# Optimization experiments

Measured on AMD Instinct MI355X. Metric: run time of the kernel, lower is better.

## Reference

```python
import jax, jax.numpy as jnp
import numpy as np

SEQ, B, IN_DIM, EMB, HID, L = 2048, 32, 512, 256, 256, 16
START, STOP = 0, 1
HH = HID // 2  # per-direction hidden size
NEG = -10000.0


def _lstm_dir(xs, Wih, Whh, b, h0, c0, reverse):
    # xs: (T, B, EMB); Wih: (4*HH, EMB); Whh: (4*HH, HH); b: (4*HH,)
    def step(carry, x):
        h, c = carry
        g = x @ Wih.T + h @ Whh.T + b  # (B, 4*HH)
        i, f, gg, o = jnp.split(g, 4, axis=-1)  # PyTorch gate order i,f,g,o
        c = jax.nn.sigmoid(f) * c + jax.nn.sigmoid(i) * jnp.tanh(gg)
        h = jax.nn.sigmoid(o) * jnp.tanh(c)
        return (h, c), h
    _, hs = jax.lax.scan(step, (h0, c0), xs, reverse=reverse)
    return hs  # (T, B, HH)


def _features(source_seq, in_W, in_b, Wih_f, Whh_f, b_f, Wih_b, Whh_b, b_b,
              out_W, out_b, h0, c0):
    x = source_seq @ in_W.T + in_b  # (T, B, EMB)
    hf = _lstm_dir(x, Wih_f, Whh_f, b_f, h0[0], c0[0], reverse=False)
    hb = _lstm_dir(x, Wih_b, Whh_b, b_b, h0[1], c0[1], reverse=True)
    h = jnp.concatenate([hf, hb], axis=-1)  # (T, B, HID)
    return h @ out_W.T + out_b  # (T, B, L)


def _viterbi(feats, transitions):
    # transitions[i, j]: score of transitioning to label i from label j
    fv = jnp.full((B, L), NEG, feats.dtype).at[:, START].set(0.0)

    def step(fv, feat):
        scores = fv[:, None, :] + transitions[None, :, :]  # (B, next, prev)
        bp = jnp.argmax(scores, axis=2).astype(jnp.int32)   # (B, L)
        fv = jnp.max(scores, axis=2) + feat
        return fv, bp

    fv, bps = jax.lax.scan(step, fv, feats)  # bps: (T, B, L)
    term = fv + transitions[STOP][None, :]   # (B, L)
    score = jnp.max(term, axis=1)            # (B,)
    best_last = jnp.argmax(term, axis=1).astype(jnp.int32)  # (B,)

    def back(lbl, bp):
        prev = jnp.take_along_axis(bp, lbl[:, None], axis=1)[:, 0]
        return prev, lbl

    _, path = jax.lax.scan(back, best_last, bps, reverse=True)  # (T, B)
    return score, path


def setup_inputs() -> dict:
    key = jax.random.key(0)
    ks = jax.random.split(key, 16)
    s = 0.05
    return {
        "source_seq": jax.random.normal(ks[0], (SEQ, B, IN_DIM), jnp.float32),
        "in_W": jax.random.normal(ks[1], (EMB, IN_DIM), jnp.float32) * s,
        "in_b": jnp.zeros((EMB,), jnp.float32),
        "Wih_f": jax.random.normal(ks[2], (4 * HH, EMB), jnp.float32) * s,
        "Whh_f": jax.random.normal(ks[3], (4 * HH, HH), jnp.float32) * s,
        "b_f": jnp.zeros((4 * HH,), jnp.float32),
        "Wih_b": jax.random.normal(ks[4], (4 * HH, EMB), jnp.float32) * s,
        "Whh_b": jax.random.normal(ks[5], (4 * HH, HH), jnp.float32) * s,
        "b_b": jnp.zeros((4 * HH,), jnp.float32),
        "out_W": jax.random.normal(ks[6], (L, HID), jnp.float32) * s,
        "out_b": jnp.zeros((L,), jnp.float32),
        "transitions": jax.random.normal(ks[7], (L, L), jnp.float32),
        "h0": jax.random.normal(ks[8], (2, B, HH), jnp.float32),
        "c0": jax.random.normal(ks[9], (2, B, HH), jnp.float32),
    }


def reference(source_seq, in_W, in_b, Wih_f, Whh_f, b_f, Wih_b, Whh_b, b_b,
              out_W, out_b, transitions, h0, c0):
    feats = _features(source_seq, in_W, in_b, Wih_f, Whh_f, b_f,
                      Wih_b, Whh_b, b_b, out_W, out_b, h0, c0)
    score, labels = _viterbi(feats, transitions)
    return score, labels
```

## Files before the change

### kernel.cpp

```cpp
#include <hip/hip_runtime.h>
#include <hip/hip_bf16.h>

typedef __attribute__((ext_vector_type(8))) short bf16x8;
typedef __attribute__((ext_vector_type(4))) float f32x4;
typedef __attribute__((ext_vector_type(4))) unsigned u32x4;
typedef __attribute__((ext_vector_type(2))) unsigned u32x2;

#define SEQT 2048
#define BATCH 32
#define INDIM 512
#define EMB 256
#define HHX 128
#define LBL 16
#define LOG2E 1.44269504f

__device__ __forceinline__ unsigned short f2bf(float f) {
    unsigned u = __float_as_uint(f);
    u += 0x7FFFu + ((u >> 16) & 1u);
    return (unsigned short)(u >> 16);
}
#define BLO(u) __uint_as_float((u) << 16)
#define BHI(u) __uint_as_float((u) & 0xffff0000u)

__device__ __forceinline__ float cell(float ig, float fg, float gg, float og, float& c) {
    float Ef = __builtin_amdgcn_exp2f(fminf(fg, 30.f));
    float Ei = __builtin_amdgcn_exp2f(fminf(ig, 30.f));
    float Eg = __builtin_amdgcn_exp2f(fminf(gg, 60.f));
    float Eo = __builtin_amdgcn_exp2f(fminf(og, 30.f));
    float pf = 1.f + Ef;
    float t1 = (Eg + 1.f) * (1.f + Ei);
    float num = c * t1 + (Eg - 1.f) * pf;
    float cn = num * __builtin_amdgcn_rcpf(pf * t1);
    c = cn;
    float E2 = __builtin_amdgcn_exp2f(fminf(2.f * LOG2E * cn, 60.f));
    float r3 = __builtin_amdgcn_rcpf((E2 + 1.f) * (1.f + Eo));
    return (E2 - 1.f) * r3;
}

__device__ __forceinline__ int orig_of(int gp) {
    return ((gp >> 4) & 3) * 128 + (gp >> 6) * 16 + (gp & 15);
}
__device__ __forceinline__ float gate_scale(int gp) {
    return (((gp >> 4) & 3) == 2) ? (2.f * LOG2E) : (-LOG2E);
}

__global__ __launch_bounds__(256) void k_prep_wc(
    const float* __restrict__ in_W, const float* __restrict__ in_b,
    const float* __restrict__ Wih_f, const float* __restrict__ b_f,
    const float* __restrict__ Wih_b, const float* __restrict__ b_b,
    unsigned short* __restrict__ Wc, float* __restrict__ bc)
{
    int G0 = blockIdx.x * 8;
    int tid = threadIdx.x;
    __shared__ float wrow[8][EMB];
    for (int e = tid; e < 8 * EMB; e += 256) {
        int r = e >> 8, ee = e & 255;
        int G = G0 + r, dir = G >> 9, gp = G & 511;
        wrow[r][ee] = (dir ? Wih_b : Wih_f)[orig_of(gp) * EMB + ee] * gate_scale(gp);
    }
    __syncthreads();
    for (int k = tid; k < INDIM; k += 256) {
        float acc[8] = {0, 0, 0, 0, 0, 0, 0, 0};
        #pragma unroll 4
        for (int e = 0; e < EMB; ++e) {
            float x = in_W[e * INDIM + k];
            #pragma unroll
            for (int r = 0; r < 8; ++r) acc[r] += wrow[r][e] * x;
        }
        #pragma unroll
        for (int r = 0; r < 8; ++r) Wc[(size_t)(G0 + r) * INDIM + k] = f2bf(acc[r]);
    }
    if (tid < 64) {
        for (int r = 0; r < 8; ++r) {
            float p = 0.f;
            for (int e = tid; e < EMB; e += 64) p += wrow[r][e] * in_b[e];
            for (int off = 32; off; off >>= 1) p += __shfl_xor(p, off);
            if (tid == 0) {
                int G = G0 + r, dir = G >> 9, gp = G & 511;
                bc[G] = (dir ? b_b : b_f)[orig_of(gp)] * gate_scale(gp) + p;
            }
        }
    }
}

__global__ __launch_bounds__(256) void k_prep_misc(
    const float* __restrict__ Whh_f, const float* __restrict__ Whh_b,
    const float* __restrict__ out_W,
    unsigned short* __restrict__ Whh_bf, unsigned short* __restrict__ outW_bf)
{
    int idx = blockIdx.x * 256 + threadIdx.x;
    int stride = gridDim.x * 256;
    for (int i = idx; i < 1024 * HHX; i += stride) {
        int G = i >> 7, k = i & 127;
        int dir = G >> 9, gp = G & 511;
        const float* Whh = dir ? Whh_b : Whh_f;
        Whh_bf[i] = f2bf(Whh[orig_of(gp) * HHX + k] * gate_scale(gp));
    }
    for (int i = idx; i < LBL * 256; i += stride) outW_bf[i] = f2bf(out_W[i]);
}

__global__ __launch_bounds__(512) void k_gemm_p(
    const float* __restrict__ S, const unsigned short* __restrict__ Wc,
    const float* __restrict__ bc, unsigned short* __restrict__ P2)
{
    int m0 = blockIdx.y * 64;
    int n0 = blockIdx.x * 256;
    int tid = threadIdx.x;
    int w = tid >> 6, l = tid & 63;
    int lr = l & 15, lq = l >> 4;
    int wm = w >> 2, wn = w & 3;

    __shared__ __align__(16) unsigned short Alds[64 * 64];
    __shared__ __align__(16) unsigned short Blds[256 * 64];

    const f32x4 fzero = {0.f, 0.f, 0.f, 0.f};
    f32x4 acc[2][4];
    #pragma unroll
    for (int a = 0; a < 2; ++a)
        #pragma unroll
        for (int b = 0; b < 4; ++b) acc[a][b] = fzero;

    for (int kt = 0; kt < 8; ++kt) {
        {
            int r = tid >> 3, c = tid & 7;
            const float* src = S + (size_t)(m0 + r) * INDIM + kt * 64 + c * 8;
            float4 v0 = *(const float4*)src;
            float4 v1 = *(const float4*)(src + 4);
            unsigned g0, g1, g2, g3;
            asm("v_cvt_pk_bf16_f32 %0, %1, %2" : "=v"(g0) : "v"(v0.x), "v"(v0.y));
            asm("v_cvt_pk_bf16_f32 %0, %1, %2" : "=v"(g1) : "v"(v0.z), "v"(v0.w));
            asm("v_cvt_pk_bf16_f32 %0, %1, %2" : "=v"(g2) : "v"(v1.x), "v"(v1.y));
            asm("v_cvt_pk_bf16_f32 %0, %1, %2" : "=v"(g3) : "v"(v1.z), "v"(v1.w));
            u32x4 wv = {g0, g1, g2, g3};
            *(u32x4*)((char*)Alds + r * 128 + ((c * 16) ^ ((r & 7) << 4))) = wv;
        }
        {
            int r = tid >> 1, h = tid & 1;
            const unsigned short* bs = Wc + (size_t)(n0 + r) * INDIM + kt * 64;
            #pragma unroll
            for (int cc = 0; cc < 4; ++cc) {
                int ch = h * 4 + cc;
                bf16x8 v = *(const bf16x8*)(bs + ch * 8);
                *(bf16x8*)((char*)Blds + r * 128 + ((ch * 16) ^ ((r & 7) << 4))) = v;
            }
        }
        __syncthreads();
        bf16x8 af[2][2], bfv[4][2];
        #pragma unroll
        for (int tm = 0; tm < 2; ++tm)
            #pragma unroll
            for (int kk = 0; kk < 2; ++kk) {
                int ra = wm * 32 + tm * 16 + lr;
                af[tm][kk] = *(const bf16x8*)((char*)Alds + ra * 128 + ((kk * 64 + lq * 16) ^ ((ra & 7) << 4)));
            }
        #pragma unroll
        for (int tn = 0; tn < 4; ++tn)
            #pragma unroll
            for (int kk = 0; kk < 2; ++kk) {
                int rb = wn * 64 + tn * 16 + lr;
                bfv[tn][kk] = *(const bf16x8*)((char*)Blds + rb * 128 + ((kk * 64 + lq * 16) ^ ((rb & 7) << 4)));
            }
        #pragma unroll
        for (int tm = 0; tm < 2; ++tm)
            #pragma unroll
            for (int tn = 0; tn < 4; ++tn)
                #pragma unroll
                for (int kk = 0; kk < 2; ++kk)
                    acc[tm][tn] = __builtin_amdgcn_mfma_f32_16x16x32_bf16(af[tm][kk], bfv[tn][kk], acc[tm][tn], 0, 0, 0);
        __syncthreads();
    }
    char* bounce = (char*)Blds;
    {
        float b4[4];
        #pragma unroll
        for (int tn = 0; tn < 4; ++tn) b4[tn] = bc[n0 + wn * 64 + tn * 16 + lr];
        int wbyte = wn * 512 + lr * 32;
        #pragma unroll
        for (int tm = 0; tm < 2; ++tm) {
            #pragma unroll
            for (int j = 0; j < 4; ++j) {
                float f0 = acc[tm][0][j] + b4[0], f1 = acc[tm][1][j] + b4[1];
                float f2 = acc[tm][2][j] + b4[2], f3 = acc[tm][3][j] + b4[3];
                unsigned pA, pB;
                asm("v_cvt_pk_bf16_f32 %0, %1, %2" : "=v"(pA) : "v"(f0), "v"(f1));
                asm("v_cvt_pk_bf16_f32 %0, %1, %2" : "=v"(pB) : "v"(f2), "v"(f3));
                *(u32x2*)(bounce + (wm * 8 + tm * 4 + lq) * 2048 + wbyte + j * 8) = (u32x2){pA, pB};
            }
        }
    }
    __syncthreads();
    {
        int dirg = blockIdx.x >> 1;
        int halfoff = (blockIdx.x & 1) * 2048;
        #pragma unroll
        for (int s = 0; s < 4; ++s) {
            int idx = tid * 4 + s;
            int fl = idx >> 7, infr = (idx & 127) * 16;
            int t = blockIdx.y * 2 + (fl >> 3), bq = fl & 7;
            u32x4 v = *(u32x4*)(bounce + idx * 16);
            char* dst = (char*)P2 + ((size_t)((t * 2 + dirg) * 8 + bq)) * 4096 + halfoff + infr;
            *(u32x4*)dst = v;
        }
    }
}

__global__ __launch_bounds__(512) void k_lstm(
    const unsigned short* __restrict__ P2, const unsigned short* __restrict__ Whh_bf,
    const float* __restrict__ h0, const float* __restrict__ c0,
    unsigned short* __restrict__ H)
{
    int blk = blockIdx.x;
    int dir = blk >> 3, bq = blk & 7;
    int tid = threadIdx.x;
    int w = tid >> 6, l = tid & 63;
    int lr = l & 15, lq = l >> 4;

    __shared__ __align__(16) unsigned short hbuf[2][2056];
    char* hb = (char*)hbuf;

    bf16x8 bfrag[4][4];
    #pragma unroll
    for (int q = 0; q < 4; ++q)
        #pragma unroll
        for (int ko = 0; ko < 4; ++ko) {
            int row = dir * 512 + w * 64 + q * 16 + lr;
            bfrag[q][ko] = *(const bf16x8*)(Whh_bf + (size_t)row * HHX + ko * 32 + lq * 8);
        }

    int u = w * 16 + lr;
    float cA = c0[(dir * 32 + bq * 4 + lq) * HHX + u];

    for (int e = tid; e < 2048; e += 512) {
        int r = e >> 7, uu = e & 127;
        unsigned short v = 0;
        if ((r & 3) == 0) v = f2bf(h0[(dir * 32 + bq * 4 + (r >> 2)) * HHX + uu]);
        int addr = (r * 256 + uu * 2) ^ ((r & 7) << 4);
        *(unsigned short*)(hb + addr) = v;
    }
    if (tid < 8) {
        *(unsigned short*)(hb + 4096 + tid * 2) = 0;
        *(unsigned short*)(hb + 4112 + 4096 + tid * 2) = 0;
    }
    __syncthreads();

    const bool zl = (lr & 3) != 0;
    const int rd0 = zl ? 4096 : ((lr * 256 + 0 * 64 + lq * 16) ^ ((lr & 7) << 4));
    const int rd1 = zl ? 4096 : ((lr * 256 + 1 * 64 + lq * 16) ^ ((lr & 7) << 4));
    const int rd2 = zl ? 4096 : ((lr * 256 + 2 * 64 + lq * 16) ^ ((lr & 7) << 4));
    const int rd3 = zl ? 4096 : ((lr * 256 + 3 * 64 + lq * 16) ^ ((lr & 7) << 4));
    const int rA = lq * 4;
    const int waA = (rA * 256 + u * 2) ^ ((rA & 7) << 4);

    int t0 = dir ? (SEQT - 1) : 0;
    const long long pstep = (dir ? -1LL : 1LL) * (2LL * 8 * 2048);
    const unsigned short* pptr = P2 + ((size_t)(t0 * 2 + dir) * 8 + bq) * 2048 + ((size_t)u * 4 + lq) * 4;
    u32x2 pc = *(const u32x2*)pptr;
    pptr += pstep;

    unsigned short* hpA = H + ((size_t)t0 * 32 + bq * 4 + lq) * 256 + dir * 128 + u;
    const long long hstep = (dir ? -1LL : 1LL) * (32 * 256);

#define LBAR() asm volatile("s_waitcnt lgkmcnt(0)\n\ts_barrier" ::: "memory")

#define STEP(CUR, PF) do { \
    bf16x8 af0 = *(const bf16x8*)(hb + (CUR) * 4112 + rd0); \
    bf16x8 af1 = *(const bf16x8*)(hb + (CUR) * 4112 + rd1); \
    bf16x8 af2 = *(const bf16x8*)(hb + (CUR) * 4112 + rd2); \
    bf16x8 af3 = *(const bf16x8*)(hb + (CUR) * 4112 + rd3); \
    u32x2 u0 = pc; \
    if (PF) { pc = *(const u32x2*)pptr; pptr += pstep; } \
    f32x4 a0 = {BLO(u0.x), 0.f, 0.f, 0.f}; \
    f32x4 a1 = {BHI(u0.x), 0.f, 0.f, 0.f}; \
    f32x4 a2 = {BLO(u0.y), 0.f, 0.f, 0.f}; \
    f32x4 a3 = {BHI(u0.y), 0.f, 0.f, 0.f}; \
    a0 = __builtin_amdgcn_mfma_f32_16x16x32_bf16(af0, bfrag[0][0], a0, 0, 0, 0); \
    a0 = __builtin_amdgcn_mfma_f32_16x16x32_bf16(af1, bfrag[0][1], a0, 0, 0, 0); \
    a0 = __builtin_amdgcn_mfma_f32_16x16x32_bf16(af2, bfrag[0][2], a0, 0, 0, 0); \
    a0 = __builtin_amdgcn_mfma_f32_16x16x32_bf16(af3, bfrag[0][3], a0, 0, 0, 0); \
    a1 = __builtin_amdgcn_mfma_f32_16x16x32_bf16(af0, bfrag[1][0], a1, 0, 0, 0); \
    a1 = __builtin_amdgcn_mfma_f32_16x16x32_bf16(af1, bfrag[1][1], a1, 0, 0, 0); \
    a1 = __builtin_amdgcn_mfma_f32_16x16x32_bf16(af2, bfrag[1][2], a1, 0, 0, 0); \
    a1 = __builtin_amdgcn_mfma_f32_16x16x32_bf16(af3, bfrag[1][3], a1, 0, 0, 0); \
    a2 = __builtin_amdgcn_mfma_f32_16x16x32_bf16(af0, bfrag[2][0], a2, 0, 0, 0); \
    a2 = __builtin_amdgcn_mfma_f32_16x16x32_bf16(af1, bfrag[2][1], a2, 0, 0, 0); \
    a2 = __builtin_amdgcn_mfma_f32_16x16x32_bf16(af2, bfrag[2][2], a2, 0, 0, 0); \
    a2 = __builtin_amdgcn_mfma_f32_16x16x32_bf16(af3, bfrag[2][3], a2, 0, 0, 0); \
    a3 = __builtin_amdgcn_mfma_f32_16x16x32_bf16(af0, bfrag[3][0], a3, 0, 0, 0); \
    a3 = __builtin_amdgcn_mfma_f32_16x16x32_bf16(af1, bfrag[3][1], a3, 0, 0, 0); \
    a3 = __builtin_amdgcn_mfma_f32_16x16x32_bf16(af2, bfrag[3][2], a3, 0, 0, 0); \
    a3 = __builtin_amdgcn_mfma_f32_16x16x32_bf16(af3, bfrag[3][3], a3, 0, 0, 0); \
    float hnA = cell(a0[0], a1[0], a2[0], a3[0], cA); \
    unsigned pk; \
    asm("v_cvt_pk_bf16_f32 %0, %1, %2" : "=v"(pk) : "v"(hnA), "v"(hnA)); \
    unsigned short sA = (unsigned short)pk; \
    *(unsigned short*)(hb + (((CUR) ^ 1) * 4112) + waA) = sA; \
    hpA[0] = sA; \
    hpA += hstep; \
    LBAR(); \
} while (0)

    for (int it = 0; it < 1023; ++it) {
        STEP(0, true);
        STEP(1, true);
    }
    STEP(0, true);
    STEP(1, false);
#undef STEP
#undef LBAR
}

__global__ __launch_bounds__(256) void k_feats(
    const unsigned short* __restrict__ H, const unsigned short* __restrict__ outW_bf,
    const float* __restrict__ out_b, float* __restrict__ feats)
{
    int m0 = blockIdx.x * 64;
    int tid = threadIdx.x;
    int w = tid >> 6, l = tid & 63;
    int lr = l & 15, lq = l >> 4;
    __shared__ __align__(16) unsigned short Hl[64 * 256];

    {
        int r = tid >> 2, cb = (tid & 3) * 8;
        #pragma unroll
        for (int cc = 0; cc < 8; ++cc) {
            int c = cb + cc;
            bf16x8 v = *(const bf16x8*)(H + (size_t)(m0 + r) * 256 + c * 8);
            *(bf16x8*)((char*)Hl + r * 512 + ((c * 16) ^ ((r & 7) << 4))) = v;
        }
    }
    bf16x8 bw[8];
    #pragma unroll
    for (int ko = 0; ko < 8; ++ko)
        bw[ko] = *(const bf16x8*)(outW_bf + lr * 256 + ko * 32 + lq * 8);
    __syncthreads();
    int row = w * 16 + lr;
    f32x4 acc = {0.f, 0.f, 0.f, 0.f};
    #pragma unroll
    for (int ko = 0; ko < 8; ++ko) {
        bf16x8 a = *(const bf16x8*)((char*)Hl + row * 512 + ((ko * 64 + lq * 16) ^ ((row & 7) << 4)));
        acc = __builtin_amdgcn_mfma_f32_16x16x32_bf16(a, bw[ko], acc, 0, 0, 0);
    }
    float ob = out_b[lr];
    #pragma unroll
    for (int j = 0; j < 4; ++j) {
        int m = m0 + w * 16 + lq * 4 + j;
        feats[(size_t)m * 16 + lr] = acc[j] + ob;
    }
}

template <int CTRL>
__device__ __forceinline__ float dppf(float x) {
    return __int_as_float(__builtin_amdgcn_update_dpp(0, __float_as_int(x), CTRL, 0xF, 0xF, true));
}
template <int CTRL>
__device__ __forceinline__ int dppi(int x) {
    return __builtin_amdgcn_update_dpp(0, x, CTRL, 0xF, 0xF, true);
}

__global__ __launch_bounds__(64) void k_viterbi(
    const float* __restrict__ feats, const float* __restrict__ trans,
    float* __restrict__ out)
{
    int b = blockIdx.x;
    int l = threadIdx.x;
    int i = l >> 2, s = l & 3;
    __shared__ unsigned char bp[SEQT * 16];
    __shared__ __align__(16) float fch[256 * 16];
    __shared__ unsigned long long bp64[SEQT];

    float tr[4];
    #pragma unroll
    for (int m = 0; m < 4; ++m) tr[m] = trans[i * 16 + s * 4 + m];
    float fvloc[4];
    #pragma unroll
    for (int m = 0; m < 4; ++m) fvloc[m] = (s * 4 + m == 0) ? 0.f : -10000.f;

    int ga[4];
    #pragma unroll
    for (int m = 0; m < 4; ++m) ga[m] = (16 * s + 4 * m) * 4;

    for (int t = 0; t < SEQT; ++t) {
        if ((t & 255) == 0) {
            __syncthreads();
            for (int k = l; k < 256; k += 64) {
                const float4* src = (const float4*)(feats + (size_t)((t + k) * 32 + b) * 16);
                float4 v0 = src[0], v1 = src[1], v2 = src[2], v3 = src[3];
                float4* dst = (float4*)(fch + k * 16);
                dst[0] = v0; dst[1] = v1; dst[2] = v2; dst[3] = v3;
            }
            __syncthreads();
        }
        float best = fvloc[0] + tr[0];
        int bj = s * 4;
        #pragma unroll
        for (int m = 1; m < 4; ++m) {
            float v = fvloc[m] + tr[m];
            if (v > best) { best = v; bj = s * 4 + m; }
        }
        {
            float ov = dppf<0xB1>(best); int oj = dppi<0xB1>(bj);
            bool take = (ov > best) || (ov == best && oj < bj);
            best = take ? ov : best; bj = take ? oj : bj;
        }
        {
            float ov = dppf<0x4E>(best); int oj = dppi<0x4E>(bj);
            bool take = (ov > best) || (ov == best && oj < bj);
            best = take ? ov : best; bj = take ? oj : bj;
        }
        float fvn = best + fch[(t & 255) * 16 + i];
        if (s == 0) bp[t * 16 + i] = (unsigned char)bj;
        #pragma unroll
        for (int m = 0; m < 4; ++m)
            fvloc[m] = __int_as_float(__builtin_amdgcn_ds_bpermute(ga[m], __float_as_int(fvn)));
    }
    float bestS = fvloc[0] + trans[16 + s * 4];
    int bl = s * 4;
    #pragma unroll
    for (int m = 1; m < 4; ++m) {
        float tv = fvloc[m] + trans[16 + s * 4 + m];
        if (tv > bestS) { bestS = tv; bl = s * 4 + m; }
    }
    {
        float ov = dppf<0xB1>(bestS); int oj = dppi<0xB1>(bl);
        bool take = (ov > bestS) || (ov == bestS && oj < bl);
        bestS = take ? ov : bestS; bl = take ? oj : bl;
    }
    {
        float ov = dppf<0x4E>(bestS); int oj = dppi<0x4E>(bl);
        bool take = (ov > bestS) || (ov == bestS && oj < bl);
        bestS = take ? ov : bestS; bl = take ? oj : bl;
    }
    __syncthreads();
    for (int t = l; t < SEQT; t += 64) {
        const uint4* p = (const uint4*)(bp + t * 16);
        uint4 u = *p;
        unsigned n0 = (u.x | (u.x >> 4)) & 0x00FF00FFu; n0 = (n0 | (n0 >> 8)) & 0xFFFFu;
        unsigned n1 = (u.y | (u.y >> 4)) & 0x00FF00FFu; n1 = (n1 | (n1 >> 8)) & 0xFFFFu;
        unsigned n2 = (u.z | (u.z >> 4)) & 0x00FF00FFu; n2 = (n2 | (n2 >> 8)) & 0xFFFFu;
        unsigned n3 = (u.w | (u.w >> 4)) & 0x00FF00FFu; n3 = (n3 | (n3 >> 8)) & 0xFFFFu;
        bp64[t] = (unsigned long long)n0 | ((unsigned long long)n1 << 16)
                | ((unsigned long long)n2 << 32) | ((unsigned long long)n3 << 48);
    }
    __syncthreads();
    if (l == 0) out[b] = bestS;
    int lbl = bl;
    #pragma unroll 8
    for (int t = SEQT - 1; t >= 0; --t) {
        if ((t & 63) == l) out[32 + (size_t)t * 32 + b] = (float)lbl;
        lbl = (int)((bp64[t] >> (lbl * 4)) & 15ull);
    }
}

extern "C" void kernel_launch(void* const* d_in, const int* in_sizes, int n_in,
                              void* d_out, int out_size, void* d_ws, size_t ws_size,
                              hipStream_t stream) {
    const float* source = (const float*)d_in[0];
    const float* in_W  = (const float*)d_in[1];
    const float* in_b  = (const float*)d_in[2];
    const float* Wih_f = (const float*)d_in[3];
    const float* Whh_f = (const float*)d_in[4];
    const float* b_f   = (const float*)d_in[5];
    const float* Wih_b = (const float*)d_in[6];
    const float* Whh_b = (const float*)d_in[7];
    const float* b_b   = (const float*)d_in[8];
    const float* out_W = (const float*)d_in[9];
    const float* out_b = (const float*)d_in[10];
    const float* trans = (const float*)d_in[11];
    const float* h0    = (const float*)d_in[12];
    const float* c0    = (const float*)d_in[13];
    float* out = (float*)d_out;

    char* ws = (char*)d_ws;
    unsigned short* P2      = (unsigned short*)(ws);
    unsigned short* H       = (unsigned short*)(ws + 134217728);
    float*          feats   = (float*)         (ws + 167772160);
    unsigned short* Wc      = (unsigned short*)(ws + 171966464);
    float*          bc      = (float*)         (ws + 173015040);
    unsigned short* Whh_bf  = (unsigned short*)(ws + 173019136);
    unsigned short* outW_bf = (unsigned short*)(ws + 173281280);

    hipLaunchKernelGGL(k_prep_wc, dim3(128), dim3(256), 0, stream,
                       in_W, in_b, Wih_f, b_f, Wih_b, b_b, Wc, bc);
    hipLaunchKernelGGL(k_prep_misc, dim3(256), dim3(256), 0, stream,
                       Whh_f, Whh_b, out_W, Whh_bf, outW_bf);
    hipLaunchKernelGGL(k_gemm_p, dim3(4, 1024), dim3(512), 0, stream,
                       source, Wc, bc, P2);
    hipLaunchKernelGGL(k_lstm, dim3(16), dim3(512), 0, stream,
                       P2, Whh_bf, h0, c0, H);
    hipLaunchKernelGGL(k_feats, dim3(1024), dim3(256), 0, stream,
                       H, outW_bf, out_b, feats);
    hipLaunchKernelGGL(k_viterbi, dim3(32), dim3(64), 0, stream,
                       feats, trans, out);
}
```

Before: 1.841 ms.

## Fuse input-projection GEMM with LSTM recurrence using per-tile readiness flags

Merges the input-projection GEMM and the LSTM recurrence into one persistent launch. The first 16 blocks run the recurrence and spin on per-time-tile atomic flags, while the remaining blocks compute P2 tiles in the order each direction consumes them and publish completion with release atomics. This is meant to overlap the long serial recurrence with the GEMM instead of waiting for the whole GEMM to finish. It also splits each gate's MFMA accumulation chain into two independent chains to shorten dependency latency. The cost is a flag memset, spin-wait polling, and reliance on the 16 LSTM blocks being scheduled alongside GEMM blocks without deadlock.

```diff
diff --git a/kernel.cpp b/kernel.cpp
--- a/kernel.cpp
+++ b/kernel.cpp
@@ -99,169 +99,73 @@
     for (int i = idx; i < LBL * 256; i += stride) outW_bf[i] = f2bf(out_W[i]);
 }
 
-__global__ __launch_bounds__(512) void k_gemm_p(
+__global__ __launch_bounds__(512) void k_fused(
     const float* __restrict__ S, const unsigned short* __restrict__ Wc,
-    const float* __restrict__ bc, unsigned short* __restrict__ P2)
+    const float* __restrict__ bc, unsigned short* __restrict__ P2,
+    const unsigned short* __restrict__ Whh_bf,
+    const float* __restrict__ h0, const float* __restrict__ c0,
+    unsigned short* __restrict__ H, unsigned* __restrict__ flags)
 {
-    int m0 = blockIdx.y * 64;
-    int n0 = blockIdx.x * 256;
+    __shared__ __align__(16) char smem[40960];
     int tid = threadIdx.x;
-    int w = tid >> 6, l = tid & 63;
-    int lr = l & 15, lq = l >> 4;
-    int wm = w >> 2, wn = w & 3;
-
-    __shared__ __align__(16) unsigned short Alds[64 * 64];
-    __shared__ __align__(16) unsigned short Blds[256 * 64];
-
-    const f32x4 fzero = {0.f, 0.f, 0.f, 0.f};
-    f32x4 acc[2][4];
-    #pragma unroll
-    for (int a = 0; a < 2; ++a)
+
+    if (blockIdx.x < 16) {
+        int blk = blockIdx.x;
+        int dir = blk >> 3, bq = blk & 7;
+        int w = tid >> 6, l = tid & 63;
+        int lr = l & 15, lq = l >> 4;
+        char* hb = smem;
+
+        bf16x8 bfrag[4][4];
         #pragma unroll
-        for (int b = 0; b < 4; ++b) acc[a][b] = fzero;
-
-    for (int kt = 0; kt < 8; ++kt) {
-        {
-            int r = tid >> 3, c = tid & 7;
-            const float* src = S + (size_t)(m0 + r) * INDIM + kt * 64 + c * 8;
-            float4 v0 = *(const float4*)src;
-            float4 v1 = *(const float4*)(src + 4);
-            unsigned g0, g1, g2, g3;
-            asm("v_cvt_pk_bf16_f32 %0, %1, %2" : "=v"(g0) : "v"(v0.x), "v"(v0.y));
-            asm("v_cvt_pk_bf16_f32 %0, %1, %2" : "=v"(g1) : "v"(v0.z), "v"(v0.w));
-            asm("v_cvt_pk_bf16_f32 %0, %1, %2" : "=v"(g2) : "v"(v1.x), "v"(v1.y));
-            asm("v_cvt_pk_bf16_f32 %0, %1, %2" : "=v"(g3) : "v"(v1.z), "v"(v1.w));
-            u32x4 wv = {g0, g1, g2, g3};
-            *(u32x4*)((char*)Alds + r * 128 + ((c * 16) ^ ((r & 7) << 4))) = wv;
-        }
-        {
-            int r = tid >> 1, h = tid & 1;
-            const unsigned short* bs = Wc + (size_t)(n0 + r) * INDIM + kt * 64;
-            #pragma unroll
-            for (int cc = 0; cc < 4; ++cc) {
-                int ch = h * 4 + cc;
-                bf16x8 v = *(const bf16x8*)(bs + ch * 8);
-                *(bf16x8*)((char*)Blds + r * 128 + ((ch * 16) ^ ((r & 7) << 4))) = v;
-            }
+        for (int q = 0; q < 4; ++q)
+            #pragma unroll
+            for (int ko = 0; ko < 4; ++ko) {
+                int row = dir * 512 + w * 64 + q * 16 + lr;
+                bfrag[q][ko] = *(const bf16x8*)(Whh_bf + (size_t)row * HHX + ko * 32 + lq * 8);
+            }
+
+        int u = w * 16 + lr;
+        float cA = c0[(dir * 32 + bq * 4 + lq) * HHX + u];
+
+        for (int e = tid; e < 2048; e += 512) {
+            int r = e >> 7, uu = e & 127;
+            unsigned short v = 0;
+            if ((r & 3) == 0) v = f2bf(h0[(dir * 32 + bq * 4 + (r >> 2)) * HHX + uu]);
+            int addr = (r * 256 + uu * 2) ^ ((r & 7) << 4);
+            *(unsigned short*)(hb + addr) = v;
+        }
+        if (tid < 8) {
+            *(unsigned short*)(hb + 4096 + tid * 2) = 0;
+            *(unsigned short*)(hb + 4112 + 4096 + tid * 2) = 0;
+        }
+
+        int g0 = dir ? 1023 : 0;
+        if (tid == 0) {
+            while (__hip_atomic_load(&flags[g0 * 2 + dir], __ATOMIC_ACQUIRE, __HIP_MEMORY_SCOPE_AGENT) < 2u)
+                __builtin_amdgcn_s_sleep(2);
         }
         __syncthreads();
-        bf16x8 af[2][2], bfv[4][2];
-        #pragma unroll
-        for (int tm = 0; tm < 2; ++tm)
-            #pragma unroll
-            for (int kk = 0; kk < 2; ++kk) {
-                int ra = wm * 32 + tm * 16 + lr;
-                af[tm][kk] = *(const bf16x8*)((char*)Alds + ra * 128 + ((kk * 64 + lq * 16) ^ ((ra & 7) << 4)));
-            }
-        #pragma unroll
-        for (int tn = 0; tn < 4; ++tn)
-            #pragma unroll
-            for (int kk = 0; kk < 2; ++kk) {
-                int rb = wn * 64 + tn * 16 + lr;
-                bfv[tn][kk] = *(const bf16x8*)((char*)Blds + rb * 128 + ((kk * 64 + lq * 16) ^ ((rb & 7) << 4)));
-            }
-        #pragma unroll
-        for (int tm = 0; tm < 2; ++tm)
-            #pragma unroll
-            for (int tn = 0; tn < 4; ++tn)
-                #pragma unroll
-                for (int kk = 0; kk < 2; ++kk)
-                    acc[tm][tn] = __builtin_amdgcn_mfma_f32_16x16x32_bf16(af[tm][kk], bfv[tn][kk], acc[tm][tn], 0, 0, 0);
-        __syncthreads();
-    }
-    char* bounce = (char*)Blds;
-    {
-        float b4[4];
-        #pragma unroll
-        for (int tn = 0; tn < 4; ++tn) b4[tn] = bc[n0 + wn * 64 + tn * 16 + lr];
-        int wbyte = wn * 512 + lr * 32;
-        #pragma unroll
-        for (int tm = 0; tm < 2; ++tm) {
-            #pragma unroll
-            for (int j = 0; j < 4; ++j) {
-                float f0 = acc[tm][0][j] + b4[0], f1 = acc[tm][1][j] + b4[1];
-                float f2 = acc[tm][2][j] + b4[2], f3 = acc[tm][3][j] + b4[3];
-                unsigned pA, pB;
-                asm("v_cvt_pk_bf16_f32 %0, %1, %2" : "=v"(pA) : "v"(f0), "v"(f1));
-                asm("v_cvt_pk_bf16_f32 %0, %1, %2" : "=v"(pB) : "v"(f2), "v"(f3));
-                *(u32x2*)(bounce + (wm * 8 + tm * 4 + lq) * 2048 + wbyte + j * 8) = (u32x2){pA, pB};
-            }
-        }
-    }
-    __syncthreads();
-    {
-        int dirg = blockIdx.x >> 1;
-        int halfoff = (blockIdx.x & 1) * 2048;
-        #pragma unroll
-        for (int s = 0; s < 4; ++s) {
-            int idx = tid * 4 + s;
-            int fl = idx >> 7, infr = (idx & 127) * 16;
-            int t = blockIdx.y * 2 + (fl >> 3), bq = fl & 7;
-            u32x4 v = *(u32x4*)(bounce + idx * 16);
-            char* dst = (char*)P2 + ((size_t)((t * 2 + dirg) * 8 + bq)) * 4096 + halfoff + infr;
-            *(u32x4*)dst = v;
-        }
-    }
-}
-
-__global__ __launch_bounds__(512) void k_lstm(
-    const unsigned short* __restrict__ P2, const unsigned short* __restrict__ Whh_bf,
-    const float* __restrict__ h0, const float* __restrict__ c0,
-    unsigned short* __restrict__ H)
-{
-    int blk = blockIdx.x;
-    int dir = blk >> 3, bq = blk & 7;
-    int tid = threadIdx.x;
-    int w = tid >> 6, l = tid & 63;
-    int lr = l & 15, lq = l >> 4;
-
-    __shared__ __align__(16) unsigned short hbuf[2][2056];
-    char* hb = (char*)hbuf;
-
-    bf16x8 bfrag[4][4];
-    #pragma unroll
-    for (int q = 0; q < 4; ++q)
-        #pragma unroll
-        for (int ko = 0; ko < 4; ++ko) {
-            int row = dir * 512 + w * 64 + q * 16 + lr;
-            bfrag[q][ko] = *(const bf16x8*)(Whh_bf + (size_t)row * HHX + ko * 32 + lq * 8);
-        }
-
-    int u = w * 16 + lr;
-    float cA = c0[(dir * 32 + bq * 4 + lq) * HHX + u];
-
-    for (int e = tid; e < 2048; e += 512) {
-        int r = e >> 7, uu = e & 127;
-        unsigned short v = 0;
-        if ((r & 3) == 0) v = f2bf(h0[(dir * 32 + bq * 4 + (r >> 2)) * HHX + uu]);
-        int addr = (r * 256 + uu * 2) ^ ((r & 7) << 4);
-        *(unsigned short*)(hb + addr) = v;
-    }
-    if (tid < 8) {
-        *(unsigned short*)(hb + 4096 + tid * 2) = 0;
-        *(unsigned short*)(hb + 4112 + 4096 + tid * 2) = 0;
-    }
-    __syncthreads();
-
-    const bool zl = (lr & 3) != 0;
-    const int rd0 = zl ? 4096 : ((lr * 256 + 0 * 64 + lq * 16) ^ ((lr & 7) << 4));
-    const int rd1 = zl ? 4096 : ((lr * 256 + 1 * 64 + lq * 16) ^ ((lr & 7) << 4));
-    const int rd2 = zl ? 4096 : ((lr * 256 + 2 * 64 + lq * 16) ^ ((lr & 7) << 4));
-    const int rd3 = zl ? 4096 : ((lr * 256 + 3 * 64 + lq * 16) ^ ((lr & 7) << 4));
-    const int rA = lq * 4;
-    const int waA = (rA * 256 + u * 2) ^ ((rA & 7) << 4);
-
-    int t0 = dir ? (SEQT - 1) : 0;
-    const long long pstep = (dir ? -1LL : 1LL) * (2LL * 8 * 2048);
-    const unsigned short* pptr = P2 + ((size_t)(t0 * 2 + dir) * 8 + bq) * 2048 + ((size_t)u * 4 + lq) * 4;
-    u32x2 pc = *(const u32x2*)pptr;
-    pptr += pstep;
-
-    unsigned short* hpA = H + ((size_t)t0 * 32 + bq * 4 + lq) * 256 + dir * 128 + u;
-    const long long hstep = (dir ? -1LL : 1LL) * (32 * 256);
+
+        const bool zl = (lr & 3) != 0;
+        const int rd0 = zl ? 4096 : ((lr * 256 + 0 * 64 + lq * 16) ^ ((lr & 7) << 4));
+        const int rd1 = zl ? 4096 : ((lr * 256 + 1 * 64 + lq * 16) ^ ((lr & 7) << 4));
+        const int rd2 = zl ? 4096 : ((lr * 256 + 2 * 64 + lq * 16) ^ ((lr & 7) << 4));
+        const int rd3 = zl ? 4096 : ((lr * 256 + 3 * 64 + lq * 16) ^ ((lr & 7) << 4));
+        const int rA = lq * 4;
+        const int waA = (rA * 256 + u * 2) ^ ((rA & 7) << 4);
+
+        int t0 = dir ? (SEQT - 1) : 0;
+        const long long pstep = (dir ? -1LL : 1LL) * (2LL * 8 * 2048);
+        const unsigned short* pptr = P2 + ((size_t)(t0 * 2 + dir) * 8 + bq) * 2048 + ((size_t)u * 4 + lq) * 4;
+        u32x2 pc = *(const u32x2*)pptr;
+        pptr += pstep;
+
+        unsigned short* hpA = H + ((size_t)t0 * 32 + bq * 4 + lq) * 256 + dir * 128 + u;
+        const long long hstep = (dir ? -1LL : 1LL) * (32 * 256);
 
 #define LBAR() asm volatile("s_waitcnt lgkmcnt(0)\n\ts_barrier" ::: "memory")
-
+#define MF(A, B, C) __builtin_amdgcn_mfma_f32_16x16x32_bf16(A, B, C, 0, 0, 0)
 #define STEP(CUR, PF) do { \
     bf16x8 af0 = *(const bf16x8*)(hb + (CUR) * 4112 + rd0); \
     bf16x8 af1 = *(const bf16x8*)(hb + (CUR) * 4112 + rd1); \
@@ -269,27 +173,21 @@
     bf16x8 af3 = *(const bf16x8*)(hb + (CUR) * 4112 + rd3); \
     u32x2 u0 = pc; \
     if (PF) { pc = *(const u32x2*)pptr; pptr += pstep; } \
+    const f32x4 zz = {0.f, 0.f, 0.f, 0.f}; \
     f32x4 a0 = {BLO(u0.x), 0.f, 0.f, 0.f}; \
     f32x4 a1 = {BHI(u0.x), 0.f, 0.f, 0.f}; \
     f32x4 a2 = {BLO(u0.y), 0.f, 0.f, 0.f}; \
     f32x4 a3 = {BHI(u0.y), 0.f, 0.f, 0.f}; \
-    a0 = __builtin_amdgcn_mfma_f32_16x16x32_bf16(af0, bfrag[0][0], a0, 0, 0, 0); \
-    a0 = __builtin_amdgcn_mfma_f32_16x16x32_bf16(af1, bfrag[0][1], a0, 0, 0, 0); \
-    a0 = __builtin_amdgcn_mfma_f32_16x16x32_bf16(af2, bfrag[0][2], a0, 0, 0, 0); \
-    a0 = __builtin_amdgcn_mfma_f32_16x16x32_bf16(af3, bfrag[0][3], a0, 0, 0, 0); \
-    a1 = __builtin_amdgcn_mfma_f32_16x16x32_bf16(af0, bfrag[1][0], a1, 0, 0, 0); \
-    a1 = __builtin_amdgcn_mfma_f32_16x16x32_bf16(af1, bfrag[1][1], a1, 0, 0, 0); \
-    a1 = __builtin_amdgcn_mfma_f32_16x16x32_bf16(af2, bfrag[1][2], a1, 0, 0, 0); \
-    a1 = __builtin_amdgcn_mfma_f32_16x16x32_bf16(af3, bfrag[1][3], a1, 0, 0, 0); \
-    a2 = __builtin_amdgcn_mfma_f32_16x16x32_bf16(af0, bfrag[2][0], a2, 0, 0, 0); \
-    a2 = __builtin_amdgcn_mfma_f32_16x16x32_bf16(af1, bfrag[2][1], a2, 0, 0, 0); \
-    a2 = __builtin_amdgcn_mfma_f32_16x16x32_bf16(af2, bfrag[2][2], a2, 0, 0, 0); \
-    a2 = __builtin_amdgcn_mfma_f32_16x16x32_bf16(af3, bfrag[2][3], a2, 0, 0, 0); \
-    a3 = __builtin_amdgcn_mfma_f32_16x16x32_bf16(af0, bfrag[3][0], a3, 0, 0, 0); \
-    a3 = __builtin_amdgcn_mfma_f32_16x16x32_bf16(af1, bfrag[3][1], a3, 0, 0, 0); \
-    a3 = __builtin_amdgcn_mfma_f32_16x16x32_bf16(af2, bfrag[3][2], a3, 0, 0, 0); \
-    a3 = __builtin_amdgcn_mfma_f32_16x16x32_bf16(af3, bfrag[3][3], a3, 0, 0, 0); \
-    float hnA = cell(a0[0], a1[0], a2[0], a3[0], cA); \
+    f32x4 b0 = zz, b1 = zz, b2 = zz, b3 = zz; \
+    a0 = MF(af0, bfrag[0][0], a0); a0 = MF(af1, bfrag[0][1], a0); \
+    b0 = MF(af2, bfrag[0][2], b0); b0 = MF(af3, bfrag[0][3], b0); \
+    a1 = MF(af0, bfrag[1][0], a1); a1 = MF(af1, bfrag[1][1], a1); \
+    b1 = MF(af2, bfrag[1][2], b1); b1 = MF(af3, bfrag[1][3], b1); \
+    a2 = MF(af0, bfrag[2][0], a2); a2 = MF(af1, bfrag[2][1], a2); \
+    b2 = MF(af2, bfrag[2][2], b2); b2 = MF(af3, bfrag[2][3], b2); \
+    a3 = MF(af0, bfrag[3][0], a3); a3 = MF(af1, bfrag[3][1], a3); \
+    b3 = MF(af2, bfrag[3][2], b3); b3 = MF(af3, bfrag[3][3], b3); \
+    float hnA = cell(a0[0] + b0[0], a1[0] + b1[0], a2[0] + b2[0], a3[0] + b3[0], cA); \
     unsigned pk; \
     asm("v_cvt_pk_bf16_f32 %0, %1, %2" : "=v"(pk) : "v"(hnA), "v"(hnA)); \
     unsigned short sA = (unsigned short)pk; \
@@ -299,14 +197,131 @@
     LBAR(); \
 } while (0)
 
-    for (int it = 0; it < 1023; ++it) {
+        for (int it = 0; it < 1023; ++it) {
+            int g = dir ? (1022 - it) : (it + 1);
+            if (tid == 0) {
+                while (__hip_atomic_load(&flags[g * 2 + dir], __ATOMIC_ACQUIRE, __HIP_MEMORY_SCOPE_AGENT) < 2u)
+                    __builtin_amdgcn_s_sleep(2);
+            }
+            STEP(0, true);
+            STEP(1, true);
+        }
         STEP(0, true);
-        STEP(1, true);
-    }
-    STEP(0, true);
-    STEP(1, false);
+        STEP(1, false);
 #undef STEP
+#undef MF
 #undef LBAR
+        return;
+    }
+
+    {
+        int gb = blockIdx.x - 16;
+        int bx = gb & 3;
+        int byr = gb >> 2;
+        int dirg = bx >> 1;
+        int by = dirg ? (1023 - byr) : byr;
+        int m0 = by * 64;
+        int n0 = bx * 256;
+        int w = tid >> 6, l = tid & 63;
+        int lr = l & 15, lq = l >> 4;
+        int wm = w >> 2, wn = w & 3;
+
+        unsigned short* Alds = (unsigned short*)smem;
+        unsigned short* Blds = (unsigned short*)(smem + 8192);
+
+        const f32x4 fzero = {0.f, 0.f, 0.f, 0.f};
+        f32x4 acc[2][4];
+        #pragma unroll
+        for (int a = 0; a < 2; ++a)
+            #pragma unroll
+            for (int b = 0; b < 4; ++b) acc[a][b] = fzero;
+
+        for (int kt = 0; kt < 8; ++kt) {
+            {
+                int r = tid >> 3, c = tid & 7;
+                const float* src = S + (size_t)(m0 + r) * INDIM + kt * 64 + c * 8;
+                float4 v0 = *(const float4*)src;
+                float4 v1 = *(const float4*)(src + 4);
+                unsigned g0, g1, g2, g3;
+                asm("v_cvt_pk_bf16_f32 %0, %1, %2" : "=v"(g0) : "v"(v0.x), "v"(v0.y));
+                asm("v_cvt_pk_bf16_f32 %0, %1, %2" : "=v"(g1) : "v"(v0.z), "v"(v0.w));
+                asm("v_cvt_pk_bf16_f32 %0, %1, %2" : "=v"(g2) : "v"(v1.x), "v"(v1.y));
+                asm("v_cvt_pk_bf16_f32 %0, %1, %2" : "=v"(g3) : "v"(v1.z), "v"(v1.w));
+                u32x4 wv = {g0, g1, g2, g3};
+                *(u32x4*)((char*)Alds + r * 128 + ((c * 16) ^ ((r & 7) << 4))) = wv;
+            }
+            {
+                int r = tid >> 1, h = tid & 1;
+                const unsigned short* bs = Wc + (size_t)(n0 + r) * INDIM + kt * 64;
+                #pragma unroll
+                for (int cc = 0; cc < 4; ++cc) {
+                    int ch = h * 4 + cc;
+                    bf16x8 v = *(const bf16x8*)(bs + ch * 8);
+                    *(bf16x8*)((char*)Blds + r * 128 + ((ch * 16) ^ ((r & 7) << 4))) = v;
+                }
+            }
+            __syncthreads();
+            bf16x8 af[2][2], bfv[4][2];
+            #pragma unroll
+            for (int tm = 0; tm < 2; ++tm)
+                #pragma unroll
+                for (int kk = 0; kk < 2; ++kk) {
+                    int ra = wm * 32 + tm * 16 + lr;
+                    af[tm][kk] = *(const bf16x8*)((char*)Alds + ra * 128 + ((kk * 64 + lq * 16) ^ ((ra & 7) << 4)));
+                }
+            #pragma unroll
+            for (int tn = 0; tn < 4; ++tn)
+                #pragma unroll
+                for (int kk = 0; kk < 2; ++kk) {
+                    int rb = wn * 64 + tn * 16 + lr;
+                    bfv[tn][kk] = *(const bf16x8*)((char*)Blds + rb * 128 + ((kk * 64 + lq * 16) ^ ((rb & 7) << 4)));
+                }
+            #pragma unroll
+            for (int tm = 0; tm < 2; ++tm)
+                #pragma unroll
+                for (int tn = 0; tn < 4; ++tn)
+                    #pragma unroll
+                    for (int kk = 0; kk < 2; ++kk)
+                        acc[tm][tn] = __builtin_amdgcn_mfma_f32_16x16x32_bf16(af[tm][kk], bfv[tn][kk], acc[tm][tn], 0, 0, 0);
+            __syncthreads();
+        }
+        char* bounce = (char*)Blds;
+        {
+            float b4[4];
+            #pragma unroll
+            for (int tn = 0; tn < 4; ++tn) b4[tn] = bc[n0 + wn * 64 + tn * 16 + lr];
+            int wbyte = wn * 512 + lr * 32;
+            #pragma unroll
+            for (int tm = 0; tm < 2; ++tm) {
+                #pragma unroll
+                for (int j = 0; j < 4; ++j) {
+                    float f0 = acc[tm][0][j] + b4[0], f1 = acc[tm][1][j] + b4[1];
+                    float f2 = acc[tm][2][j] + b4[2], f3 = acc[tm][3][j] + b4[3];
+                    unsigned pA, pB;
+                    asm("v_cvt_pk_bf16_f32 %0, %1, %2" : "=v"(pA) : "v"(f0), "v"(f1));
+                    asm("v_cvt_pk_bf16_f32 %0, %1, %2" : "=v"(pB) : "v"(f2), "v"(f3));
+                    *(u32x2*)(bounce + (wm * 8 + tm * 4 + lq) * 2048 + wbyte + j * 8) = (u32x2){pA, pB};
+                }
+            }
+        }
+        __syncthreads();
+        {
+            int halfoff = (bx & 1) * 2048;
+            #pragma unroll
+            for (int s = 0; s < 4; ++s) {
+                int idx = tid * 4 + s;
+                int fl = idx >> 7, infr = (idx & 127) * 16;
+                int t = by * 2 + (fl >> 3), bq = fl & 7;
+                u32x4 v = *(u32x4*)(bounce + idx * 16);
+                char* dst = (char*)P2 + ((size_t)((t * 2 + dirg) * 8 + bq)) * 4096 + halfoff + infr;
+                *(u32x4*)dst = v;
+            }
+        }
+        __threadfence();
+        __syncthreads();
+        if (tid == 0)
+            __hip_atomic_fetch_add(&flags[by * 2 + dirg], 1u, __ATOMIC_RELEASE, __HIP_MEMORY_SCOPE_AGENT);
+    }
 }
 
 __global__ __launch_bounds__(256) void k_feats(
@@ -478,15 +493,15 @@
     float*          bc      = (float*)         (ws + 173015040);
     unsigned short* Whh_bf  = (unsigned short*)(ws + 173019136);
     unsigned short* outW_bf = (unsigned short*)(ws + 173281280);
-
+    unsigned*       flags   = (unsigned*)      (ws + 173289472);
+
+    hipMemsetAsync(flags, 0, 2048 * sizeof(unsigned), stream);
     hipLaunchKernelGGL(k_prep_wc, dim3(128), dim3(256), 0, stream,
                        in_W, in_b, Wih_f, b_f, Wih_b, b_b, Wc, bc);
     hipLaunchKernelGGL(k_prep_misc, dim3(256), dim3(256), 0, stream,
                        Whh_f, Whh_b, out_W, Whh_bf, outW_bf);
-    hipLaunchKernelGGL(k_gemm_p, dim3(4, 1024), dim3(512), 0, stream,
-                       source, Wc, bc, P2);
-    hipLaunchKernelGGL(k_lstm, dim3(16), dim3(512), 0, stream,
-                       P2, Whh_bf, h0, c0, H);
+    hipLaunchKernelGGL(k_fused, dim3(16 + 4096), dim3(512), 0, stream,
+                       source, Wc, bc, P2, Whh_bf, h0, c0, H, flags);
     hipLaunchKernelGGL(k_feats, dim3(1024), dim3(256), 0, stream,
                        H, outW_bf, out_b, feats);
     hipLaunchKernelGGL(k_viterbi, dim3(32), dim3(64), 0, stream,
```

After: 3.105 ms. +68.7%, slower.
